# Kernel tuning notes

Measured on AMD Instinct MI355X. Metric: run time of the kernel, lower is better.

Reference implementation:

```python
import jax, jax.numpy as jnp
import numpy as np

B, L, H, V = 16, 512, 256, 32000
HALF = H // 2
EPS_LN = 1e-5
EPS_NORM = 1e-12


def setup_inputs() -> dict:
    key = jax.random.key(0)
    ks = jax.random.split(key, 9)
    s = 0.02
    return {
        "seq": jax.random.randint(ks[0], (B, L), 0, V),
        "embed": jax.random.normal(ks[1], (V, H), jnp.float32) * s,
        "W1": jax.random.normal(ks[2], (2 * H, H), jnp.float32) * s,
        "b1": jnp.zeros((2 * H,), jnp.float32),
        "W2": jax.random.normal(ks[3], (H, 2 * H), jnp.float32) * s,
        "b2": jnp.zeros((H,), jnp.float32),
        "gamma": jnp.ones((H,), jnp.float32),
        "beta": jnp.zeros((H,), jnp.float32),
        "W_sem": jax.random.normal(ks[4], (HALF, H), jnp.float32) * s,
        "W_epi": jax.random.normal(ks[5], (HALF, H), jnp.float32) * s,
        "W_rp": jax.random.normal(ks[6], (H, H), jnp.float32) * s,
        "b_rp": jnp.zeros((H,), jnp.float32),
        "W_out": jax.random.normal(ks[7], (V, H), jnp.float32) * s,
        "b_out": jnp.zeros((V,), jnp.float32),
    }


def _l2norm(x):
    # F.normalize(dim=-1): x / max(||x||, eps)
    n = jnp.sqrt(jnp.sum(x * x, axis=-1, keepdims=True))
    return x / jnp.maximum(n, EPS_NORM)


def reference(seq, embed, W1, b1, W2, b2, gamma, beta, W_sem, W_epi, W_rp, b_rp, W_out, b_out):
    h = embed[seq]                                   # [B, L, H]
    ff = jnp.maximum(h @ W1.T + b1, 0.0) @ W2.T + b2  # MLP with 2H hidden
    x = h + ff
    mu = jnp.mean(x, axis=-1, keepdims=True)
    var = jnp.var(x, axis=-1, keepdims=True)
    h = (x - mu) / jnp.sqrt(var + EPS_LN) * gamma + beta  # LayerNorm

    ks_all = jnp.einsum('blh,kh->blk', h, W_sem)     # [B, L, HALF]
    ke_all = jnp.einsum('blh,kh->blk', h, W_epi)

    def step(carry, kv):
        M_s, M_e = carry
        k_s, k_e = kv                                 # [B, HALF] each
        kns = _l2norm(k_s)
        kne = _l2norm(k_e)
        vps = jnp.einsum('bij,bj->bi', M_s, kns)      # read from fast weights
        vpe = jnp.einsum('bij,bj->bi', M_e, kne)
        M_s = M_s + jnp.einsum('bi,bj->bij', k_s - vps, kns)  # delta-rule write
        M_e = M_e + jnp.einsum('bi,bj->bij', k_e - vpe, kne)
        return (M_s, M_e), None

    M0 = jnp.zeros((B, HALF, HALF), h.dtype)
    # scan over timesteps 0..L-2 (time-major)
    (M_s, M_e), _ = jax.lax.scan(
        step, (M0, M0),
        (jnp.swapaxes(ks_all[:, :-1], 0, 1), jnp.swapaxes(ke_all[:, :-1], 0, 1)))

    cs = jnp.einsum('bij,bj->bi', M_s, ks_all[:, -1])  # read with last-token query
    ce = jnp.einsum('bij,bj->bi', M_e, ke_all[:, -1])
    c = jnp.concatenate([cs, ce], axis=-1)             # [B, H]
    r = c @ W_rp.T + b_rp
    return r @ W_out.T + b_out                          # [B, V]
```

## Files before the change

### kernel.cpp

```cpp
#include <hip/hip_runtime.h>

#define B_ 16
#define L_ 512
#define H_ 256
#define V_ 32000
#define HALF_ 128

typedef __attribute__((ext_vector_type(8))) short short8;
typedef __attribute__((ext_vector_type(4))) float floatx4;

__device__ __forceinline__ unsigned short f2bf(float x) {
  unsigned int u = __float_as_uint(x);
  unsigned int r = (u + 0x7FFFu + ((u >> 16) & 1u)) >> 16;
  return (unsigned short)r;
}

template <int CTRL>
__device__ __forceinline__ float dpp_xor_add(float x) {
  int y = __builtin_amdgcn_mov_dpp(__float_as_int(x), CTRL, 0xf, 0xf, true);
  return x + __int_as_float(y);
}

__device__ __forceinline__ float redu16(float p) {
  p = dpp_xor_add<0xB1>(p);
  p = dpp_xor_add<0x4E>(p);
  p = dpp_xor_add<0x141>(p);
  p = dpp_xor_add<0x140>(p);
  return p;
}

__device__ __forceinline__ void async_cp16(const float* g, float* l) {
  __builtin_amdgcn_global_load_lds(
      (const __attribute__((address_space(1))) void*)g,
      (__attribute__((address_space(3))) void*)l, 16, 0, 0);
}

__device__ __forceinline__ float dot8(const float* a, const float* b) {
  float t0 = a[0] * b[0] + a[1] * b[1];
  float t1 = a[2] * b[2] + a[3] * b[3];
  float t2 = a[4] * b[4] + a[5] * b[5];
  float t3 = a[6] * b[6] + a[7] * b[7];
  return (t0 + t1) + (t2 + t3);
}

__global__ __launch_bounds__(256) void prep_kernel(const int* __restrict__ seq,
                                                   const float* __restrict__ embed,
                                                   float* __restrict__ h,
                                                   unsigned short* __restrict__ hbf,
                                                   const float* __restrict__ W1,
                                                   const float* __restrict__ W2,
                                                   const float* __restrict__ Ws,
                                                   const float* __restrict__ We,
                                                   unsigned short* __restrict__ W1b,
                                                   unsigned short* __restrict__ W2b,
                                                   unsigned short* __restrict__ Wcb) {
  int blk = blockIdx.x;
  int tid = threadIdx.x;
  if (blk < 2048) {
    int token = blk * 4 + (tid >> 6);
    int lane = tid & 63;
    int row = seq[token];
    float4 v = ((const float4*)(embed + (size_t)row * H_))[lane];
    ((float4*)(h + (size_t)token * H_))[lane] = v;
    ushort4 o;
    o.x = f2bf(v.x); o.y = f2bf(v.y); o.z = f2bf(v.z); o.w = f2bf(v.w);
    *(ushort4*)(hbf + (size_t)token * H_ + lane * 4) = o;
  } else {
    int i = (blk - 2048) * 256 + tid;
    if (i < 131072) W1b[i] = f2bf(W1[i]);
    else if (i < 262144) W2b[i - 131072] = f2bf(W2[i - 131072]);
    else if (i < 294912) Wcb[i - 262144] = f2bf(Ws[i - 262144]);
    else Wcb[i - 262144] = f2bf(We[i - 294912]);
  }
}

template <int MT, bool RELU, bool BIAS, bool RES, bool OUT_BF16>
__global__ __launch_bounds__(256) void gemm_mfma(const unsigned short* __restrict__ A,
                                                 const unsigned short* __restrict__ Bw,
                                                 const float* __restrict__ bias,
                                                 const float* __restrict__ Res,
                                                 float* __restrict__ Cf,
                                                 unsigned short* __restrict__ Cb,
                                                 int M, int N, int K) {
  constexpr int FI = MT / 32;
  __shared__ unsigned short As[MT * 40];
  __shared__ unsigned short Bs[128 * 40];
  int tid = threadIdx.x;
  int wave = tid >> 6, lane = tid & 63;
  int wm = (wave >> 1) * (MT / 2), wn = (wave & 1) * 64;
  int quad = lane >> 4, l15 = lane & 15;
  int bm = blockIdx.y * MT, bn = blockIdx.x * 128;
  int sr = tid >> 2, sq = tid & 3;

  floatx4 zero = {0.f, 0.f, 0.f, 0.f};
  floatx4 acc[FI][4];
#pragma unroll
  for (int fi = 0; fi < FI; fi++)
#pragma unroll
    for (int fj = 0; fj < 4; fj++) acc[fi][fj] = zero;

  uint4 av0, av1, bv0, bv1;
  av0 = *(const uint4*)(A + (size_t)(bm + sr) * K + sq * 8);
  if (MT == 128) av1 = *(const uint4*)(A + (size_t)(bm + 64 + sr) * K + sq * 8);
  bv0 = *(const uint4*)(Bw + (size_t)(bn + sr) * K + sq * 8);
  bv1 = *(const uint4*)(Bw + (size_t)(bn + 64 + sr) * K + sq * 8);

  for (int k0 = 0; k0 < K; k0 += 32) {
    __syncthreads();
    *(uint4*)(As + sr * 40 + sq * 8) = av0;
    if (MT == 128) *(uint4*)(As + (64 + sr) * 40 + sq * 8) = av1;
    *(uint4*)(Bs + sr * 40 + sq * 8) = bv0;
    *(uint4*)(Bs + (64 + sr) * 40 + sq * 8) = bv1;
    __syncthreads();
    if (k0 + 32 < K) {
      av0 = *(const uint4*)(A + (size_t)(bm + sr) * K + k0 + 32 + sq * 8);
      if (MT == 128) av1 = *(const uint4*)(A + (size_t)(bm + 64 + sr) * K + k0 + 32 + sq * 8);
      bv0 = *(const uint4*)(Bw + (size_t)(bn + sr) * K + k0 + 32 + sq * 8);
      bv1 = *(const uint4*)(Bw + (size_t)(bn + 64 + sr) * K + k0 + 32 + sq * 8);
    }
    short8 af[FI], bf[4];
#pragma unroll
    for (int f = 0; f < FI; f++) af[f] = *(const short8*)(As + (wm + f * 16 + l15) * 40 + quad * 8);
#pragma unroll
    for (int f = 0; f < 4; f++) bf[f] = *(const short8*)(Bs + (wn + f * 16 + l15) * 40 + quad * 8);
#pragma unroll
    for (int fi = 0; fi < FI; fi++)
#pragma unroll
      for (int fj = 0; fj < 4; fj++)
        acc[fi][fj] = __builtin_amdgcn_mfma_f32_16x16x32_bf16(af[fi], bf[fj], acc[fi][fj], 0, 0, 0);
  }

#pragma unroll
  for (int fi = 0; fi < FI; fi++) {
#pragma unroll
    for (int fj = 0; fj < 4; fj++) {
      int col = bn + wn + fj * 16 + l15;
      float bb = BIAS ? bias[col] : 0.f;
#pragma unroll
      for (int rg = 0; rg < 4; rg++) {
        int row = bm + wm + fi * 16 + quad * 4 + rg;
        float v = acc[fi][fj][rg] + bb;
        if (RES) v += Res[(size_t)row * N + col];
        if (RELU) v = fmaxf(v, 0.f);
        if (OUT_BF16) Cb[(size_t)row * N + col] = f2bf(v);
        else Cf[(size_t)row * N + col] = v;
      }
    }
  }
}

__global__ void ln_kernel(const float* __restrict__ x, const float* __restrict__ gamma,
                          const float* __restrict__ beta, unsigned short* __restrict__ yb) {
  int row = blockIdx.x;
  int lane = threadIdx.x;
  float4 v = ((const float4*)(x + (size_t)row * H_))[lane];
  float s = v.x + v.y + v.z + v.w;
  float sq = v.x * v.x + v.y * v.y + v.z * v.z + v.w * v.w;
#pragma unroll
  for (int off = 32; off >= 1; off >>= 1) {
    s += __shfl_xor(s, off);
    sq += __shfl_xor(sq, off);
  }
  float mu = s * (1.f / H_);
  float var = sq * (1.f / H_) - mu * mu;
  float inv = rsqrtf(var + 1e-5f);
  float4 g = ((const float4*)gamma)[lane];
  float4 b = ((const float4*)beta)[lane];
  ushort4 o;
  o.x = f2bf((v.x - mu) * inv * g.x + b.x);
  o.y = f2bf((v.y - mu) * inv * g.y + b.y);
  o.z = f2bf((v.z - mu) * inv * g.z + b.z);
  o.w = f2bf((v.w - mu) * inv * g.w + b.w);
  *(ushort4*)(yb + (size_t)row * H_ + lane * 4) = o;
}

__global__ __launch_bounds__(256) void kproj_kernel(const unsigned short* __restrict__ hnb,
                                                    const unsigned short* __restrict__ Wcb,
                                                    float* __restrict__ khat,
                                                    float* __restrict__ kT) {
  __shared__ unsigned short As[32 * 40];
  __shared__ unsigned short Bs[256 * 40];
  int tid = threadIdx.x;
  int wave = tid >> 6, lane = tid & 63;
  int wm = (wave >> 1) * 16, wnh = wave & 1, wn = wnh * 128;
  int quad = lane >> 4, l15 = lane & 15;
  int bm = blockIdx.x * 32;

  floatx4 zero = {0.f, 0.f, 0.f, 0.f};
  floatx4 acc[8];
#pragma unroll
  for (int fj = 0; fj < 8; fj++) acc[fj] = zero;

  int sr = tid >> 2, sq = tid & 3;
  uint4 av, bv[4];
  if (tid < 128) av = *(const uint4*)(hnb + (size_t)(bm + sr) * H_ + sq * 8);
#pragma unroll
  for (int q = 0; q < 4; q++) {
    int unit = q * 256 + tid;
    bv[q] = *(const uint4*)(Wcb + (size_t)(unit >> 2) * H_ + (unit & 3) * 8);
  }

  for (int k0 = 0; k0 < 256; k0 += 32) {
    __syncthreads();
    if (tid < 128) *(uint4*)(As + sr * 40 + sq * 8) = av;
#pragma unroll
    for (int q = 0; q < 4; q++) {
      int unit = q * 256 + tid;
      *(uint4*)(Bs + (unit >> 2) * 40 + (unit & 3) * 8) = bv[q];
    }
    __syncthreads();
    if (k0 + 32 < 256) {
      if (tid < 128) av = *(const uint4*)(hnb + (size_t)(bm + sr) * H_ + k0 + 32 + sq * 8);
#pragma unroll
      for (int q = 0; q < 4; q++) {
        int unit = q * 256 + tid;
        bv[q] = *(const uint4*)(Wcb + (size_t)(unit >> 2) * H_ + k0 + 32 + (unit & 3) * 8);
      }
    }
    short8 af = *(const short8*)(As + (wm + l15) * 40 + quad * 8);
    short8 bf[8];
#pragma unroll
    for (int fj = 0; fj < 8; fj++)
      bf[fj] = *(const short8*)(Bs + (wn + fj * 16 + l15) * 40 + quad * 8);
#pragma unroll
    for (int fj = 0; fj < 8; fj++)
      acc[fj] = __builtin_amdgcn_mfma_f32_16x16x32_bf16(af, bf[fj], acc[fj], 0, 0, 0);
  }

  int b = bm >> 9;
  int idxm = b * 2 + wnh;
  int tloc0 = (bm & 511) + wm + quad * 4;
  float inv[4];
#pragma unroll
  for (int rg = 0; rg < 4; rg++) {
    float ssq = 0.f;
#pragma unroll
    for (int fj = 0; fj < 8; fj++) ssq += acc[fj][rg] * acc[fj][rg];
    ssq = redu16(ssq);
    inv[rg] = 1.f / fmaxf(sqrtf(ssq), 1e-12f);
  }
#pragma unroll
  for (int fj = 0; fj < 8; fj++) {
    int ch = fj * 16 + l15;
    int j = ch >> 2, e = ch & 3;
    int pj = (j & 1) ? (16 + (j >> 1)) : (j >> 1);
    int pcol = pj * 4 + e;
#pragma unroll
    for (int rg = 0; rg < 4; rg++)
      khat[((size_t)idxm * L_ + tloc0 + rg) * HALF_ + pcol] = acc[fj][rg] * inv[rg];
    float4 raw = {acc[fj][0], acc[fj][1], acc[fj][2], acc[fj][3]};
    *(float4*)(kT + (size_t)idxm * (HALF_ * L_) + (size_t)ch * L_ + tloc0) = raw;
  }
}


#define LOADPK(P, TL)                                                          \
  do {                                                                         \
    _Pragma("unroll") for (int u_ = 0; u_ < 4; u_++) {                         \
      *(float4*)&P[u_][0] = *(const float4*)(base + ((TL) + u_) * 128);        \
      *(float4*)&P[u_][4] = *(const float4*)(base + ((TL) + u_) * 128 + 64);   \
    }                                                                          \
  } while (0)

#define GRP4(P, PN, TL, DOLOAD)                                                \
  do {                                                                         \
    if (DOLOAD) LOADPK(PN, (TL) + 4);                                          \
    float4 krc_ = *(const float4*)(krp + (TL));                                \
    float4 aA_ = *(const float4*)&a_s[(TL) >> 2][0];                           \
    float2 aB_ = *(const float2*)&a_s[(TL) >> 2][4];                           \
    float P0_ = redu16(dot8(m, P[0]));                                         \
    float P1_ = redu16(dot8(m, P[1]));                                         \
    float P2_ = redu16(dot8(m, P[2]));                                         \
    float P3_ = redu16(dot8(m, P[3]));                                         \
    float s0_ = krc_.x - P0_;                                                  \
    float s1_ = (krc_.y - P1_) - s0_ * aA_.x;                                  \
    float s2_ = (krc_.z - P2_) - (s0_ * aA_.y + s1_ * aA_.z);                  \
    float s3_ = (krc_.w - P3_) - ((s0_ * aA_.w + s1_ * aB_.x) + s2_ * aB_.y);  \
    _Pragma("unroll") for (int j_ = 0; j_ < 8; j_++) {                         \
      float mm_ = m[j_];                                                       \
      mm_ += s0_ * P[0][j_];                                                   \
      mm_ += s1_ * P[1][j_];                                                   \
      mm_ += s2_ * P[2][j_];                                                   \
      mm_ += s3_ * P[3][j_];                                                   \
      m[j_] = mm_;                                                             \
    }                                                                          \
  } while (0)

__global__ __launch_bounds__(256) void scan_kernel(const float* __restrict__ khat,
                                                   const float* __restrict__ kT,
                                                   float* __restrict__ c) {
  __shared__ float sk[2][64 * 128];
  __shared__ float krs[16 * 520];
  __shared__ float a_s[16][8];
  int bid = blockIdx.x;
  int idxm = bid & 31;
  int rg = bid >> 5;
  int b = idxm >> 1, mat = idxm & 1;
  const float* kh = khat + (size_t)idxm * L_ * HALF_;
  const float* kTi = kT + (size_t)idxm * HALF_ * L_;

  int tid = threadIdx.x;
  int wv = tid >> 6, ln = tid & 63;
  int seg = tid & 15, rl = tid >> 4;
  int r = rg * 16 + rl;
  int c0 = seg * 8;

  float m[8];
#pragma unroll
  for (int g = 0; g < 8; g++) m[g] = 0.f;

  {
    const float* gk = kTi + (size_t)rg * 16 * 512;
    float4 krv[8];
#pragma unroll
    for (int j = 0; j < 8; j++) krv[j] = *(const float4*)(gk + wv * 2048 + j * 256 + ln * 4);
    const float* g0 = kh + wv * 2048 + ln * 4;
    float* l0 = &sk[0][wv * 2048];
#pragma unroll
    for (int j = 0; j < 8; j++) async_cp16(g0 + j * 256, l0 + j * 256);
#pragma unroll
    for (int j = 0; j < 8; j++) {
      int idx = wv * 2048 + j * 256 + ln * 4;
      *(float4*)(krs + (idx >> 9) * 520 + (idx & 511)) = krv[j];
    }
  }
  __syncthreads();

  for (int ch = 0; ch < 8; ch++) {
    if (ch < 7) {
      const float* gs = kh + (size_t)(ch + 1) * 8192 + wv * 2048 + ln * 4;
      float* ls = &sk[(ch + 1) & 1][wv * 2048];
#pragma unroll
      for (int j = 0; j < 8; j++) async_cp16(gs + j * 256, ls + j * 256);
    }
    const float* base = &sk[ch & 1][0] + seg * 4;
    {
      float kv[4][8];
#pragma unroll
      for (int u = 0; u < 4; u++) {
        *(float4*)&kv[u][0] = *(const float4*)(base + (rl * 4 + u) * 128);
        *(float4*)&kv[u][4] = *(const float4*)(base + (rl * 4 + u) * 128 + 64);
      }
      float d10 = redu16(dot8(kv[1], kv[0]));
      float d20 = redu16(dot8(kv[2], kv[0]));
      float d21 = redu16(dot8(kv[2], kv[1]));
      float d30 = redu16(dot8(kv[3], kv[0]));
      float d31 = redu16(dot8(kv[3], kv[1]));
      float d32 = redu16(dot8(kv[3], kv[2]));
      if (seg == 0) {
        a_s[rl][0] = d10; a_s[rl][1] = d20; a_s[rl][2] = d21;
        a_s[rl][3] = d30; a_s[rl][4] = d31; a_s[rl][5] = d32;
      }
    }
    __syncthreads();

    const float* krp = krs + rl * 520 + ch * 64;
    float pA[4][8], pB[4][8];
    LOADPK(pA, 0);
    for (int g = 0; g < 7; g++) {
      GRP4(pA, pB, g * 8, 1);
      GRP4(pB, pA, g * 8 + 4, 1);
    }
    GRP4(pA, pB, 56, 1);
    if (ch < 7) {
      GRP4(pB, pA, 60, 0);
    } else {
      float4 krc = *(const float4*)(krp + 60);
      float4 aA = *(const float4*)&a_s[15][0];
      float P0 = redu16(dot8(m, pB[0]));
      float P1 = redu16(dot8(m, pB[1]));
      float P2 = redu16(dot8(m, pB[2]));
      float s0 = krc.x - P0;
      float s1 = (krc.y - P1) - s0 * aA.x;
      float s2 = (krc.z - P2) - (s0 * aA.y + s1 * aA.z);
#pragma unroll
      for (int j = 0; j < 8; j++)
        m[j] += s0 * pB[0][j] + s1 * pB[1][j] + s2 * pB[2][j];
    }
    __syncthreads();
  }

  float q[8];
#pragma unroll
  for (int j = 0; j < 8; j++) q[j] = kTi[(size_t)(c0 + j) * L_ + 511];
  float p = redu16(dot8(m, q));
  if (seg == 0) c[(size_t)b * H_ + mat * HALF_ + r] = p;
}

__global__ void rp_kernel(const float* __restrict__ c, const float* __restrict__ Wrp,
                          const float* __restrict__ brp, float* __restrict__ r) {
  int b = blockIdx.x;
  int n = threadIdx.x;
  __shared__ float cs[H_];
  cs[n] = c[(size_t)b * H_ + n];
  __syncthreads();
  const float4* w4 = (const float4*)(Wrp + (size_t)n * H_);
  const float4* c4 = (const float4*)cs;
  float acc = 0.f;
#pragma unroll 8
  for (int k = 0; k < H_ / 4; k++) {
    float4 w = w4[k], cc = c4[k];
    acc += w.x * cc.x + w.y * cc.y + w.z * cc.z + w.w * cc.w;
  }
  r[(size_t)b * H_ + n] = acc + brp[n];
}

__global__ __launch_bounds__(256) void out_kernel(const float* __restrict__ r,
                                                  const float* __restrict__ Wout,
                                                  const float* __restrict__ bout,
                                                  float* __restrict__ out) {
  __shared__ float rs[16 * 272];
  __shared__ float obuf[16 * 68];
  int tid = threadIdx.x;
#pragma unroll
  for (int q = 0; q < 16; q++) {
    int idx = q * 256 + tid;
    int bb = idx >> 8, cc = idx & 255;
    rs[bb * 272 + cc + 4 * (cc >> 6)] = r[idx];
  }
  __syncthreads();
  int row = tid >> 2, part = tid & 3;
  int v = blockIdx.x * 64 + row;
  const float4* w4 = (const float4*)(Wout + (size_t)v * H_ + part * 64);
  float acc[16];
#pragma unroll
  for (int bb = 0; bb < 16; bb++) acc[bb] = 0.f;
#pragma unroll 4
  for (int j = 0; j < 16; j++) {
    float4 w = w4[j];
#pragma unroll
    for (int bb = 0; bb < 16; bb++) {
      float4 rv = *(const float4*)&rs[bb * 272 + part * 68 + j * 4];
      acc[bb] += w.x * rv.x + w.y * rv.y + w.z * rv.z + w.w * rv.w;
    }
  }
  float bo = bout[v];
#pragma unroll
  for (int bb = 0; bb < 16; bb++) {
    acc[bb] = dpp_xor_add<0xB1>(acc[bb]);
    acc[bb] = dpp_xor_add<0x4E>(acc[bb]);
  }
#pragma unroll
  for (int q = 0; q < 4; q++) {
    int bb = part * 4 + q;
    obuf[bb * 68 + row] = acc[bb] + bo;
  }
  __syncthreads();
#pragma unroll
  for (int q = 0; q < 4; q++) {
    int idx = q * 256 + tid;
    int bb = idx >> 6, vl = idx & 63;
    out[(size_t)bb * V_ + blockIdx.x * 64 + vl] = obuf[bb * 68 + vl];
  }
}

extern "C" void kernel_launch(void* const* d_in, const int* in_sizes, int n_in,
                              void* d_out, int out_size, void* d_ws, size_t ws_size,
                              hipStream_t stream) {
  const int* seq = (const int*)d_in[0];
  const float* embed = (const float*)d_in[1];
  const float* W1 = (const float*)d_in[2];
  const float* b1 = (const float*)d_in[3];
  const float* W2 = (const float*)d_in[4];
  const float* b2 = (const float*)d_in[5];
  const float* gamma = (const float*)d_in[6];
  const float* beta = (const float*)d_in[7];
  const float* Wsem = (const float*)d_in[8];
  const float* Wepi = (const float*)d_in[9];
  const float* Wrp = (const float*)d_in[10];
  const float* brp = (const float*)d_in[11];
  const float* Wout = (const float*)d_in[12];
  const float* bout = (const float*)d_in[13];
  float* out = (float*)d_out;

  float* ws = (float*)d_ws;
  float* h = ws;
  float* kT = ws;
  unsigned short* a1b = (unsigned short*)(ws + 2097152);
  float* khat = ws + 2097152;
  unsigned short* hbf = (unsigned short*)(ws + 4194304);
  unsigned short* hnb = (unsigned short*)(ws + 5242880);
  unsigned short* W1b = (unsigned short*)(ws + 6291456);
  unsigned short* W2b = (unsigned short*)(ws + 6356992);
  unsigned short* Wcb = (unsigned short*)(ws + 6422528);
  float* c = ws + 6455296;
  float* r = ws + 6459392;

  prep_kernel<<<3328, 256, 0, stream>>>(seq, embed, h, hbf, W1, W2, Wsem, Wepi, W1b, W2b, Wcb);
  gemm_mfma<128, true, true, false, true><<<dim3(4, 64), 256, 0, stream>>>(
      hbf, W1b, b1, nullptr, nullptr, a1b, 8192, 512, 256);
  gemm_mfma<64, false, true, true, false><<<dim3(2, 128), 256, 0, stream>>>(
      a1b, W2b, b2, h, h, nullptr, 8192, 256, 512);
  ln_kernel<<<8192, 64, 0, stream>>>(h, gamma, beta, hnb);
  kproj_kernel<<<256, 256, 0, stream>>>(hnb, Wcb, khat, kT);
  scan_kernel<<<256, 256, 0, stream>>>(khat, kT, c);
  rp_kernel<<<16, 256, 0, stream>>>(c, Wrp, brp, r);
  out_kernel<<<500, 256, 0, stream>>>(r, Wout, bout, out);
}
```

Before: 232.3 us.

## Pipeline delta-rule scan by precomputing cross-group key dots to decouple M update

```diff
diff --git a/kernel.cpp b/kernel.cpp
--- a/kernel.cpp
+++ b/kernel.cpp
@@ -36,11 +36,15 @@
 }
 
 __device__ __forceinline__ float dot8(const float* a, const float* b) {
-  float t0 = a[0] * b[0] + a[1] * b[1];
-  float t1 = a[2] * b[2] + a[3] * b[3];
-  float t2 = a[4] * b[4] + a[5] * b[5];
-  float t3 = a[6] * b[6] + a[7] * b[7];
-  return (t0 + t1) + (t2 + t3);
+  float acc = a[0] * b[0];
+  acc = fmaf(a[1], b[1], acc);
+  acc = fmaf(a[2], b[2], acc);
+  acc = fmaf(a[3], b[3], acc);
+  acc = fmaf(a[4], b[4], acc);
+  acc = fmaf(a[5], b[5], acc);
+  acc = fmaf(a[6], b[6], acc);
+  acc = fmaf(a[7], b[7], acc);
+  return acc;
 }
 
 __global__ __launch_bounds__(256) void prep_kernel(const int* __restrict__ seq,
@@ -262,28 +266,32 @@
     }                                                                          \
   } while (0)
 
-#define GRP4(P, PN, TL, DOLOAD)                                                \
+#define ITER3(A, B, C, g, DOLOAD)                                              \
   do {                                                                         \
-    if (DOLOAD) LOADPK(PN, (TL) + 4);                                          \
-    float4 krc_ = *(const float4*)(krp + (TL));                                \
-    float4 aA_ = *(const float4*)&a_s[(TL) >> 2][0];                           \
-    float2 aB_ = *(const float2*)&a_s[(TL) >> 2][4];                           \
-    float P0_ = redu16(dot8(m, P[0]));                                         \
-    float P1_ = redu16(dot8(m, P[1]));                                         \
-    float P2_ = redu16(dot8(m, P[2]));                                         \
-    float P3_ = redu16(dot8(m, P[3]));                                         \
-    float s0_ = krc_.x - P0_;                                                  \
-    float s1_ = (krc_.y - P1_) - s0_ * aA_.x;                                  \
-    float s2_ = (krc_.z - P2_) - (s0_ * aA_.y + s1_ * aA_.z);                  \
-    float s3_ = (krc_.w - P3_) - ((s0_ * aA_.w + s1_ * aB_.x) + s2_ * aB_.y);  \
-    _Pragma("unroll") for (int j_ = 0; j_ < 8; j_++) {                         \
-      float mm_ = m[j_];                                                       \
-      mm_ += s0_ * P[0][j_];                                                   \
-      mm_ += s1_ * P[1][j_];                                                   \
-      mm_ += s2_ * P[2][j_];                                                   \
-      mm_ += s3_ * P[3][j_];                                                   \
-      m[j_] = mm_;                                                             \
-    }                                                                          \
+    if (DOLOAD) LOADPK(C, ((g) + 2) * 4);                                      \
+    float4 krn_ = *(const float4*)(krp + ((g) + 1) * 4);                       \
+    float4 aA_ = *(const float4*)&a_s[(g) + 1][0];                             \
+    float2 aB_ = *(const float2*)&a_s[(g) + 1][4];                             \
+    float4 c0_ = *(const float4*)&c_s[g][0];                                   \
+    float4 c1_ = *(const float4*)&c_s[g][4];                                   \
+    float4 c2_ = *(const float4*)&c_s[g][8];                                   \
+    float4 c3_ = *(const float4*)&c_s[g][12];                                  \
+    float D0_ = redu16(dot8(m, B[0]));                                         \
+    float D1_ = redu16(dot8(m, B[1]));                                         \
+    float D2_ = redu16(dot8(m, B[2]));                                         \
+    float D3_ = redu16(dot8(m, B[3]));                                         \
+    _Pragma("unroll") for (int j_ = 0; j_ < 8; j_++)                           \
+      m[j_] += s[0] * A[0][j_] + s[1] * A[1][j_] + s[2] * A[2][j_] +           \
+               s[3] * A[3][j_];                                                \
+    float e0_ = krn_.x - ((s[0] * c0_.x + s[1] * c0_.y) + (s[2] * c0_.z + s[3] * c0_.w)); \
+    float e1_ = krn_.y - ((s[0] * c1_.x + s[1] * c1_.y) + (s[2] * c1_.z + s[3] * c1_.w)); \
+    float e2_ = krn_.z - ((s[0] * c2_.x + s[1] * c2_.y) + (s[2] * c2_.z + s[3] * c2_.w)); \
+    float e3_ = krn_.w - ((s[0] * c3_.x + s[1] * c3_.y) + (s[2] * c3_.z + s[3] * c3_.w)); \
+    float t0_ = e0_ - D0_;                                                     \
+    float t1_ = (e1_ - D1_) - t0_ * aA_.x;                                     \
+    float t2_ = (e2_ - D2_) - (t0_ * aA_.y + t1_ * aA_.z);                     \
+    float t3_ = (e3_ - D3_) - ((t0_ * aA_.w + t1_ * aB_.x) + t2_ * aB_.y);     \
+    s[0] = t0_; s[1] = t1_; s[2] = t2_; s[3] = t3_;                            \
   } while (0)
 
 __global__ __launch_bounds__(256) void scan_kernel(const float* __restrict__ khat,
@@ -292,6 +300,7 @@
   __shared__ float sk[2][64 * 128];
   __shared__ float krs[16 * 520];
   __shared__ float a_s[16][8];
+  __shared__ float c_s[16][16];
   int bid = blockIdx.x;
   int idxm = bid & 31;
   int rg = bid >> 5;
@@ -334,12 +343,14 @@
       for (int j = 0; j < 8; j++) async_cp16(gs + j * 256, ls + j * 256);
     }
     const float* base = &sk[ch & 1][0] + seg * 4;
+
     {
-      float kv[4][8];
-#pragma unroll
-      for (int u = 0; u < 4; u++) {
-        *(float4*)&kv[u][0] = *(const float4*)(base + (rl * 4 + u) * 128);
-        *(float4*)&kv[u][4] = *(const float4*)(base + (rl * 4 + u) * 128 + 64);
+      float kv[8][8];
+#pragma unroll
+      for (int u = 0; u < 8; u++) {
+        int row = (rl * 4 + u) & 63;
+        *(float4*)&kv[u][0] = *(const float4*)(base + row * 128);
+        *(float4*)&kv[u][4] = *(const float4*)(base + row * 128 + 64);
       }
       float d10 = redu16(dot8(kv[1], kv[0]));
       float d20 = redu16(dot8(kv[2], kv[0]));
@@ -347,35 +358,56 @@
       float d30 = redu16(dot8(kv[3], kv[0]));
       float d31 = redu16(dot8(kv[3], kv[1]));
       float d32 = redu16(dot8(kv[3], kv[2]));
+      float cx[4][4];
+#pragma unroll
+      for (int u = 0; u < 4; u++)
+#pragma unroll
+        for (int v = 0; v < 4; v++) cx[u][v] = redu16(dot8(kv[4 + u], kv[v]));
       if (seg == 0) {
         a_s[rl][0] = d10; a_s[rl][1] = d20; a_s[rl][2] = d21;
         a_s[rl][3] = d30; a_s[rl][4] = d31; a_s[rl][5] = d32;
+#pragma unroll
+        for (int u = 0; u < 4; u++)
+#pragma unroll
+          for (int v = 0; v < 4; v++) c_s[rl][u * 4 + v] = cx[u][v];
       }
     }
     __syncthreads();
 
     const float* krp = krs + rl * 520 + ch * 64;
-    float pA[4][8], pB[4][8];
-    LOADPK(pA, 0);
-    for (int g = 0; g < 7; g++) {
-      GRP4(pA, pB, g * 8, 1);
-      GRP4(pB, pA, g * 8 + 4, 1);
-    }
-    GRP4(pA, pB, 56, 1);
+    float P[4][8], PN[4][8], PF[4][8], s[4];
+    LOADPK(P, 0);
+    LOADPK(PN, 4);
+    {
+      float4 kr0 = *(const float4*)(krp);
+      float4 aA = *(const float4*)&a_s[0][0];
+      float2 aB = *(const float2*)&a_s[0][4];
+      float D0 = redu16(dot8(m, P[0]));
+      float D1 = redu16(dot8(m, P[1]));
+      float D2 = redu16(dot8(m, P[2]));
+      float D3 = redu16(dot8(m, P[3]));
+      s[0] = kr0.x - D0;
+      s[1] = (kr0.y - D1) - s[0] * aA.x;
+      s[2] = (kr0.z - D2) - (s[0] * aA.y + s[1] * aA.z);
+      s[3] = (kr0.w - D3) - ((s[0] * aA.w + s[1] * aB.x) + s[2] * aB.y);
+    }
+    for (int g3 = 0; g3 < 4; g3++) {
+      int g = g3 * 3;
+      ITER3(P, PN, PF, g, 1);
+      ITER3(PN, PF, P, g + 1, 1);
+      ITER3(PF, P, PN, g + 2, 1);
+    }
+    ITER3(P, PN, PF, 12, 1);
+    ITER3(PN, PF, P, 13, 1);
+    ITER3(PF, P, PN, 14, 0);
     if (ch < 7) {
-      GRP4(pB, pA, 60, 0);
+#pragma unroll
+      for (int j = 0; j < 8; j++)
+        m[j] += s[0] * P[0][j] + s[1] * P[1][j] + s[2] * P[2][j] + s[3] * P[3][j];
     } else {
-      float4 krc = *(const float4*)(krp + 60);
-      float4 aA = *(const float4*)&a_s[15][0];
-      float P0 = redu16(dot8(m, pB[0]));
-      float P1 = redu16(dot8(m, pB[1]));
-      float P2 = redu16(dot8(m, pB[2]));
-      float s0 = krc.x - P0;
-      float s1 = (krc.y - P1) - s0 * aA.x;
-      float s2 = (krc.z - P2) - (s0 * aA.y + s1 * aA.z);
 #pragma unroll
       for (int j = 0; j < 8; j++)
-        m[j] += s0 * pB[0][j] + s1 * pB[1][j] + s2 * pB[2][j];
+        m[j] += s[0] * P[0][j] + s[1] * P[1][j] + s[2] * P[2][j];
     }
     __syncthreads();
   }
```

Result: slower. 243.2 us (+4.7%).
